# Optimization experiments

Measured on AMD Instinct MI355X. Metric: run time of the kernel, lower is better.

The kernel has to match this reference:

```python
import jax, jax.numpy as jnp
import numpy as np

PERI_IDX = np.array([0, 1, 2, 3, 5, 6, 7, 8])  # non-center taps of the 3x3 window


def _extract_patches(x, stride, padding):
    # x: [B,C,H,W] -> patches [B,C,9,Hout,Wout], tap k = di*3+dj (row-major), matching F.unfold.
    B, C, H, W = x.shape
    Hout = (H + 2 * padding - 3) // stride + 1
    Wout = (W + 2 * padding - 3) // stride + 1
    xp = jnp.pad(x, ((0, 0), (0, 0), (padding, padding), (padding, padding)))
    taps = [xp[:, :, di:di + (Hout - 1) * stride + 1:stride, dj:dj + (Wout - 1) * stride + 1:stride]
            for di in range(3) for dj in range(3)]
    return jnp.stack(taps, axis=2)  # [B,C,9,Hout,Wout]


def setup_inputs() -> dict:
    key = jax.random.key(0)
    k1, k2, k3, k4 = jax.random.split(key, 4)
    B, C, O, H, W = 8, 64, 64, 128, 128
    x = jax.random.normal(k1, (B, C, H, W), dtype=jnp.float32)
    core = jax.random.normal(k2, (O, C, 1, 1), dtype=jnp.float32) * (1.0 / np.sqrt(C))
    periphery = jax.random.uniform(k3, (8,), dtype=jnp.float32, minval=-0.1, maxval=0.1)
    threshold = jnp.array([0.1], dtype=jnp.float32)
    scale = jnp.array([10.0], dtype=jnp.float32)
    return {"x": x, "core": core, "periphery": periphery, "threshold": threshold,
            "scale": scale, "stride": 1, "padding": 1}


def reference(x, core, periphery, threshold, scale, stride, padding):
    B, C, H, W = x.shape
    O = core.shape[0]
    patches = _extract_patches(x, stride, padding)           # [B,C,9,Ho,Wo]
    center = patches[:, :, 4]                                 # [B,C,Ho,Wo]
    # per-pixel variance-like routing statistic over channels and taps
    div = jnp.sum((patches - center[:, :, None]) ** 2, axis=(1, 2))  # [B,Ho,Wo]
    m_hard = jax.nn.sigmoid((div - threshold[0]) * scale[0]) > 0.5   # [B,Ho,Wo] bool
    w = core.reshape(O, C)
    # path 0 (low variance): 1x1 conv on the center pixel
    zero_out = jnp.einsum('bchw,oc->bohw', center, w)
    # path 1 (high variance): periphery-weighted sum then 1x1 conv
    agg = jnp.einsum('bckhw,k->bchw', patches[:, :, PERI_IDX], periphery)
    one_out = jnp.einsum('bchw,oc->bohw', agg, w)
    return jnp.where(m_hard[:, None], one_out, zero_out)
```

## Files before the change

kernel.cpp:

```cpp
#include <hip/hip_runtime.h>
#include <hip/hip_bf16.h>

constexpr int Bc = 8;
constexpr int Cc = 64;
constexpr int Oc = 64;
constexpr int Hc = 128;
constexpr int Wc = 128;
constexpr int HWc = Hc * Wc;
constexpr int CP = 72;

typedef __attribute__((ext_vector_type(8))) short short8;
typedef __attribute__((ext_vector_type(4))) float floatx4;

__global__ __launch_bounds__(512) void spconv_kernel(
    const float* __restrict__ x, const float* __restrict__ core,
    const float* __restrict__ peri, const float* __restrict__ thr,
    const float* __restrict__ scl, float* __restrict__ out)
{
    __shared__ __hip_bfloat16 s_selT[Wc][CP];
    __shared__ __hip_bfloat16 s_core[Oc][CP];
    __shared__ float s_divp[4][Wc];
    __shared__ float s_msk[Wc];

    const int tid = threadIdx.x;
    const int w   = tid & (Wc - 1);
    const int q   = tid >> 7;
    const int b   = blockIdx.x >> 7;
    const int h   = blockIdx.x & (Hc - 1);

    #pragma unroll
    for (int i = 0; i < 8; ++i) {
        const int idx = i * 512 + tid;
        s_core[idx >> 6][idx & 63] = __float2bfloat16(core[idx]);
    }

    const float* xb = x + (size_t)b * Cc * HWc + (size_t)h * Wc;

    const int   dh[8] = {-1,-1,-1, 0, 0, 1, 1, 1};
    const int   dw[8] = {-1, 0, 1,-1, 1,-1, 0, 1};
    int   off[8];
    float pl[8], mf[8];
    #pragma unroll
    for (int k = 0; k < 8; ++k) {
        const bool okh = (h + dh[k] >= 0) && (h + dh[k] < Hc);
        const bool okw = (w + dw[k] >= 0) && (w + dw[k] < Wc);
        const bool ok  = okh && okw;
        off[k] = ok ? (w + dh[k] * Wc + dw[k]) : w;
        mf[k]  = ok ? 1.f : 0.f;
        pl[k]  = ok ? peri[k] : 0.f;
    }

    float divacc = 0.f;
    const float* rowq = xb + (size_t)(q * 16) * HWc;
    #pragma unroll 4
    for (int ci = 0; ci < 16; ++ci) {
        const float* row = rowq + (size_t)ci * HWc;
        const float t4 = row[w];
        float v[8];
        #pragma unroll
        for (int k = 0; k < 8; ++k) v[k] = row[off[k]];
        float agg = 0.f;
        #pragma unroll
        for (int k = 0; k < 8; ++k) agg = fmaf(pl[k], v[k], agg);
        s_selT[w][q * 16 + ci] = __float2bfloat16(agg);
        #pragma unroll
        for (int k = 0; k < 8; ++k) {
            const float d = fmaf(mf[k], v[k], -t4);
            divacc = fmaf(d, d, divacc);
        }
    }
    s_divp[q][w] = divacc;
    __syncthreads();

    if (tid < Wc) {
        const float div = s_divp[0][tid] + s_divp[1][tid]
                        + s_divp[2][tid] + s_divp[3][tid];
        s_msk[tid] = (((div - thr[0]) * scl[0]) > 0.f) ? 1.f : 0.f;
    }
    __syncthreads();

    #pragma unroll
    for (int i = 0; i < 16; ++i) {
        const int idx = i * 512 + tid;
        const int ww  = idx & (Wc - 1);
        const int c   = idx >> 7;
        if (s_msk[ww] == 0.f)
            s_selT[ww][c] = __float2bfloat16(xb[(size_t)c * HWc + ww]);
    }
    __syncthreads();

    const int lane = tid & 63;
    const int wid  = tid >> 6;
    const int o0   = (wid & 3) * 16;
    const int wh   = wid >> 2;
    const int n    = lane & 15;
    const int quad = lane >> 4;

    const short8 a0 = *(const short8*)&s_core[o0 + n][quad * 8];
    const short8 a1 = *(const short8*)&s_core[o0 + n][quad * 8 + 32];

    float* outb = out + ((size_t)(b * Oc) * Hc + h) * Wc;

    #pragma unroll
    for (int t = 0; t < 4; ++t) {
        const int w0 = (wh * 4 + t) * 16;
        const short8 b0 = *(const short8*)&s_selT[w0 + n][quad * 8];
        const short8 b1 = *(const short8*)&s_selT[w0 + n][quad * 8 + 32];
        floatx4 acc = {0.f, 0.f, 0.f, 0.f};
        acc = __builtin_amdgcn_mfma_f32_16x16x32_bf16(a0, b0, acc, 0, 0, 0);
        acc = __builtin_amdgcn_mfma_f32_16x16x32_bf16(a1, b1, acc, 0, 0, 0);
        #pragma unroll
        for (int r = 0; r < 4; ++r) {
            const int o = o0 + quad * 4 + r;
            outb[(size_t)o * HWc + w0 + n] = acc[r];
        }
    }
}

extern "C" void kernel_launch(void* const* d_in, const int* in_sizes, int n_in,
                              void* d_out, int out_size, void* d_ws, size_t ws_size,
                              hipStream_t stream) {
    const float* x    = (const float*)d_in[0];
    const float* core = (const float*)d_in[1];
    const float* peri = (const float*)d_in[2];
    const float* thr  = (const float*)d_in[3];
    const float* scl  = (const float*)d_in[4];
    float* out = (float*)d_out;

    spconv_kernel<<<dim3(Bc * Hc), dim3(512), 0, stream>>>(
        x, core, peri, thr, scl, out);
}
```

Measured before the change: 106.6 us.

## Vectorize stencil loads with float4 and shuffles, swizzle shared layout

Each thread now handles 4 adjacent columns for 4 channels, loading the three rows as float4 and getting the halo neighbours through warp shuffles instead of 9 scalar gathers per channel. The transposed bf16 tile in shared memory uses an XOR swizzle to cut bank conflicts on the packed stores and the MFMA operand reads. Core weights are loaded with vector loads and the launch bound requests 4 blocks per CU. The per-thread register footprint grows, and the divergence partial sums now need 16 partial rows reduced instead of 4.

```diff
diff --git a/kernel.cpp b/kernel.cpp
--- a/kernel.cpp
+++ b/kernel.cpp
@@ -10,72 +10,113 @@
 constexpr int CP = 72;
 
 typedef __attribute__((ext_vector_type(8))) short short8;
+typedef __attribute__((ext_vector_type(4))) short short4v;
 typedef __attribute__((ext_vector_type(4))) float floatx4;
 
-__global__ __launch_bounds__(512) void spconv_kernel(
+__device__ __forceinline__ int swz(int w, int c) {
+    return ((((c >> 3) ^ (w >> 2)) & 7) << 3) | (c & 7);
+}
+
+__device__ __forceinline__ short f2bf(float f) {
+    __hip_bfloat16 h = __float2bfloat16(f);
+    return *reinterpret_cast<short*>(&h);
+}
+
+__global__ __launch_bounds__(512, 4) void spconv_kernel(
     const float* __restrict__ x, const float* __restrict__ core,
     const float* __restrict__ peri, const float* __restrict__ thr,
     const float* __restrict__ scl, float* __restrict__ out)
 {
     __shared__ __hip_bfloat16 s_selT[Wc][CP];
     __shared__ __hip_bfloat16 s_core[Oc][CP];
-    __shared__ float s_divp[4][Wc];
+    __shared__ float s_divp[16][Wc];
     __shared__ float s_msk[Wc];
 
     const int tid = threadIdx.x;
-    const int w   = tid & (Wc - 1);
-    const int q   = tid >> 7;
+    const int wg  = tid & 31;
+    const int cg  = tid >> 5;
+    const int w0  = wg * 4;
+    const int c0  = cg * 4;
     const int b   = blockIdx.x >> 7;
     const int h   = blockIdx.x & (Hc - 1);
 
     #pragma unroll
-    for (int i = 0; i < 8; ++i) {
-        const int idx = i * 512 + tid;
-        s_core[idx >> 6][idx & 63] = __float2bfloat16(core[idx]);
+    for (int i = 0; i < 2; ++i) {
+        const int idx = (i * 512 + tid) * 4;
+        const floatx4 cv = *(const floatx4*)&core[idx];
+        short4v cv16 = { f2bf(cv.x), f2bf(cv.y), f2bf(cv.z), f2bf(cv.w) };
+        *(short4v*)&s_core[idx >> 6][idx & 63] = cv16;
     }
 
     const float* xb = x + (size_t)b * Cc * HWc + (size_t)h * Wc;
+    const bool hm = (h > 0), hp = (h < Hc - 1);
 
-    const int   dh[8] = {-1,-1,-1, 0, 0, 1, 1, 1};
-    const int   dw[8] = {-1, 0, 1,-1, 1,-1, 0, 1};
-    int   off[8];
-    float pl[8], mf[8];
+    float p[8];
     #pragma unroll
-    for (int k = 0; k < 8; ++k) {
-        const bool okh = (h + dh[k] >= 0) && (h + dh[k] < Hc);
-        const bool okw = (w + dw[k] >= 0) && (w + dw[k] < Wc);
-        const bool ok  = okh && okw;
-        off[k] = ok ? (w + dh[k] * Wc + dw[k]) : w;
-        mf[k]  = ok ? 1.f : 0.f;
-        pl[k]  = ok ? peri[k] : 0.f;
+    for (int k = 0; k < 8; ++k) p[k] = peri[k];
+
+    float div4[4] = {0.f, 0.f, 0.f, 0.f};
+    float aggv[4][4];
+    const floatx4 zero4 = {0.f, 0.f, 0.f, 0.f};
+
+    #pragma unroll
+    for (int ch = 0; ch < 4; ++ch) {
+        const float* row = xb + (size_t)(c0 + ch) * HWc;
+        const floatx4 tc = hm ? *(const floatx4*)(row - Wc + w0) : zero4;
+        const floatx4 mc =      *(const floatx4*)(row      + w0);
+        const floatx4 bc = hp ? *(const floatx4*)(row + Wc + w0) : zero4;
+
+        float tl = __shfl_up(tc.w, 1, 32),  tr = __shfl_down(tc.x, 1, 32);
+        float ml = __shfl_up(mc.w, 1, 32),  mr = __shfl_down(mc.x, 1, 32);
+        float bl = __shfl_up(bc.w, 1, 32),  br = __shfl_down(bc.x, 1, 32);
+        if (wg == 0)  { tl = 0.f; ml = 0.f; bl = 0.f; }
+        if (wg == 31) { tr = 0.f; mr = 0.f; br = 0.f; }
+
+        const float top[6] = {tl, tc.x, tc.y, tc.z, tc.w, tr};
+        const float mid[6] = {ml, mc.x, mc.y, mc.z, mc.w, mr};
+        const float bot[6] = {bl, bc.x, bc.y, bc.z, bc.w, br};
+
+        #pragma unroll
+        for (int j = 0; j < 4; ++j) {
+            const float t4 = mid[j + 1];
+            float a = p[0] * top[j];
+            a = fmaf(p[1], top[j + 1], a);
+            a = fmaf(p[2], top[j + 2], a);
+            a = fmaf(p[3], mid[j],     a);
+            a = fmaf(p[4], mid[j + 2], a);
+            a = fmaf(p[5], bot[j],     a);
+            a = fmaf(p[6], bot[j + 1], a);
+            a = fmaf(p[7], bot[j + 2], a);
+            aggv[ch][j] = a;
+
+            float s = div4[j], d;
+            d = top[j]     - t4; s = fmaf(d, d, s);
+            d = top[j + 1] - t4; s = fmaf(d, d, s);
+            d = top[j + 2] - t4; s = fmaf(d, d, s);
+            d = mid[j]     - t4; s = fmaf(d, d, s);
+            d = mid[j + 2] - t4; s = fmaf(d, d, s);
+            d = bot[j]     - t4; s = fmaf(d, d, s);
+            d = bot[j + 1] - t4; s = fmaf(d, d, s);
+            d = bot[j + 2] - t4; s = fmaf(d, d, s);
+            div4[j] = s;
+        }
     }
 
-    float divacc = 0.f;
-    const float* rowq = xb + (size_t)(q * 16) * HWc;
-    #pragma unroll 4
-    for (int ci = 0; ci < 16; ++ci) {
-        const float* row = rowq + (size_t)ci * HWc;
-        const float t4 = row[w];
-        float v[8];
-        #pragma unroll
-        for (int k = 0; k < 8; ++k) v[k] = row[off[k]];
-        float agg = 0.f;
-        #pragma unroll
-        for (int k = 0; k < 8; ++k) agg = fmaf(pl[k], v[k], agg);
-        s_selT[w][q * 16 + ci] = __float2bfloat16(agg);
-        #pragma unroll
-        for (int k = 0; k < 8; ++k) {
-            const float d = fmaf(mf[k], v[k], -t4);
-            divacc = fmaf(d, d, divacc);
-        }
+    #pragma unroll
+    for (int j = 0; j < 4; ++j) {
+        short4v av = { f2bf(aggv[0][j]), f2bf(aggv[1][j]),
+                       f2bf(aggv[2][j]), f2bf(aggv[3][j]) };
+        *(short4v*)&s_selT[w0 + j][swz(w0 + j, c0)] = av;
     }
-    s_divp[q][w] = divacc;
+    floatx4 dv4 = {div4[0], div4[1], div4[2], div4[3]};
+    *(floatx4*)&s_divp[cg][w0] = dv4;
     __syncthreads();
 
     if (tid < Wc) {
-        const float div = s_divp[0][tid] + s_divp[1][tid]
-                        + s_divp[2][tid] + s_divp[3][tid];
-        s_msk[tid] = (((div - thr[0]) * scl[0]) > 0.f) ? 1.f : 0.f;
+        float dv = 0.f;
+        #pragma unroll
+        for (int g = 0; g < 16; ++g) dv += s_divp[g][tid];
+        s_msk[tid] = (((dv - thr[0]) * scl[0]) > 0.f) ? 1.f : 0.f;
     }
     __syncthreads();
 
@@ -85,7 +126,7 @@
         const int ww  = idx & (Wc - 1);
         const int c   = idx >> 7;
         if (s_msk[ww] == 0.f)
-            s_selT[ww][c] = __float2bfloat16(xb[(size_t)c * HWc + ww]);
+            s_selT[ww][swz(ww, c)] = __float2bfloat16(xb[(size_t)c * HWc + ww]);
     }
     __syncthreads();
 
@@ -103,16 +144,16 @@
 
     #pragma unroll
     for (int t = 0; t < 4; ++t) {
-        const int w0 = (wh * 4 + t) * 16;
-        const short8 b0 = *(const short8*)&s_selT[w0 + n][quad * 8];
-        const short8 b1 = *(const short8*)&s_selT[w0 + n][quad * 8 + 32];
+        const int wq = (wh * 4 + t) * 16 + n;
+        const short8 b0 = *(const short8*)&s_selT[wq][swz(wq, quad * 8)];
+        const short8 b1 = *(const short8*)&s_selT[wq][swz(wq, quad * 8 + 32)];
         floatx4 acc = {0.f, 0.f, 0.f, 0.f};
         acc = __builtin_amdgcn_mfma_f32_16x16x32_bf16(a0, b0, acc, 0, 0, 0);
         acc = __builtin_amdgcn_mfma_f32_16x16x32_bf16(a1, b1, acc, 0, 0, 0);
         #pragma unroll
         for (int r = 0; r < 4; ++r) {
             const int o = o0 + quad * 4 + r;
-            outb[(size_t)o * HWc + w0 + n] = acc[r];
+            outb[(size_t)o * HWc + wq] = acc[r];
         }
     }
 }
```

Result: slower. 110.4 us (+3.6%).
